# Optimization experiments

Measured on AMD Instinct MI355X. Metric: run time of the kernel, lower is better.

The kernel has to match this reference:

```python
import jax, jax.numpy as jnp
import numpy as np

B, D, E, H, OUT = 4096, 1024, 8, 4096, 1024


def setup_inputs() -> dict:
    key = jax.random.key(0)
    ks = jax.random.split(key, 8)
    s_in = 1.0 / np.sqrt(D)
    s_h = 1.0 / np.sqrt(H)
    return {
        "x": jax.random.normal(ks[0], (B, D), dtype=jnp.float32),
        "Wg": jax.random.uniform(ks[1], (D, E), minval=-s_in, maxval=s_in, dtype=jnp.float32),
        "bg": jnp.zeros((E,), dtype=jnp.float32),
        "W1": jax.random.uniform(ks[2], (E, D, H), minval=-s_in, maxval=s_in, dtype=jnp.float32),
        "b1": jnp.zeros((E, H), dtype=jnp.float32),
        "W2": jax.random.uniform(ks[3], (E, H, OUT), minval=-s_h, maxval=s_h, dtype=jnp.float32),
        "b2": jnp.zeros((E, OUT), dtype=jnp.float32),
        "w_bal": jnp.float32(0.01),
    }


def reference(x, Wg, bg, W1, b1, W2, b2, w_bal):
    # Gating: softmax then top-1 (== argmax of logits)
    gate_logits = x @ Wg + bg                      # [B, E]
    assign = jnp.argmax(gate_logits, axis=1)       # [B] top-1 expert
    onehot = jax.nn.one_hot(assign, E, dtype=x.dtype)  # [B, E] dispatch mask

    # Dense dispatch: run every expert MLP, combine by one-hot (top-1 select).
    # Original returns raw expert output (no gate-prob scaling).
    h = jax.nn.relu(jnp.einsum("bd,edh->ebh", x, W1) + b1[:, None, :])  # [E, B, H]
    y = jnp.einsum("ebh,eho->ebo", h, W2) + b2[:, None, :]              # [E, B, OUT]
    output = jnp.einsum("ebo,be->bo", y, onehot)                        # [B, OUT]

    # Load-balance loss on per-expert token counts
    loads = onehot.sum(axis=0)                     # [E]
    balance_loss = jnp.sum((loads - loads.mean()) ** 2) / E
    return output, balance_loss * w_bal
```

## Files before the change

kernel.cpp:

```cpp
#include <hip/hip_runtime.h>
#include <hip/hip_bf16.h>

typedef unsigned short u16;
typedef __attribute__((ext_vector_type(8))) short bf16x8;
typedef __attribute__((ext_vector_type(4))) float f32x4;

#define BTOK 4096
#define DDIM 1024
#define NEXP 8
#define HDIM 4096
#define ODIM 1024
#define MAXTILES 40
#define MAXROWS (MAXTILES * 128)

__device__ __forceinline__ u16 f2bf(float f) {
  unsigned u = __float_as_uint(f);
  return (u16)((u + 0x7FFFu + ((u >> 16) & 1u)) >> 16);
}
__device__ __forceinline__ u16 cvt_bf(float f) {
  __hip_bfloat16 h = __float2bfloat16(f);
  u16 r;
  __builtin_memcpy(&r, &h, 2);
  return r;
}

__device__ __forceinline__ void gload16(const void* g, void* l) {
  __builtin_amdgcn_global_load_lds(
      (const __attribute__((address_space(1))) void*)g,
      (__attribute__((address_space(3))) void*)l, 16, 0, 0);
}

__global__ __launch_bounds__(256) void init_kernel(int* __restrict__ ctrl,
                                                   int* __restrict__ rowmap) {
  int i = blockIdx.x * 256 + threadIdx.x;
  if (i < 1024)
    ctrl[i] = 0;
  else
    rowmap[i - 1024] = -1;
}

__global__ __launch_bounds__(256) void gate_kernel(
    const float* __restrict__ x, const float* __restrict__ Wg,
    const float* __restrict__ bg, int* __restrict__ assign,
    int* __restrict__ counts) {
  int wave = threadIdx.x >> 6;
  int lane = threadIdx.x & 63;
  int b = blockIdx.x * 4 + wave;
  const float* xr = x + (size_t)b * DDIM;
  double acc[NEXP];
#pragma unroll
  for (int e = 0; e < NEXP; ++e) acc[e] = 0.0;
  for (int d = lane; d < DDIM; d += 64) {
    float xv = xr[d];
    const float4* wrow = (const float4*)(Wg + d * NEXP);
    float4 w0 = wrow[0], w1 = wrow[1];
    acc[0] += (double)xv * (double)w0.x;
    acc[1] += (double)xv * (double)w0.y;
    acc[2] += (double)xv * (double)w0.z;
    acc[3] += (double)xv * (double)w0.w;
    acc[4] += (double)xv * (double)w1.x;
    acc[5] += (double)xv * (double)w1.y;
    acc[6] += (double)xv * (double)w1.z;
    acc[7] += (double)xv * (double)w1.w;
  }
#pragma unroll
  for (int e = 0; e < NEXP; ++e) {
    double v = acc[e];
#pragma unroll
    for (int off = 32; off > 0; off >>= 1) v += __shfl_xor(v, off);
    acc[e] = v;
  }
  if (lane == 0) {
    int best = 0;
    double bv = acc[0] + (double)bg[0];
#pragma unroll
    for (int e = 1; e < NEXP; ++e) {
      double v = acc[e] + (double)bg[e];
      if (v > bv) { bv = v; best = e; }
    }
    assign[b] = best;
    atomicAdd(&counts[best], 1);
  }
}

__global__ void setup_kernel(const int* __restrict__ counts,
                             const float* __restrict__ wbal,
                             int* __restrict__ offp, int* __restrict__ tile_e,
                             int* __restrict__ tile_m, int* __restrict__ meta,
                             float* __restrict__ loss_out) {
  if (threadIdx.x != 0 || blockIdx.x != 0) return;
  int off = 0, nt = 0;
  for (int e = 0; e < NEXP; ++e) {
    offp[e] = off;
    int pc = (counts[e] + 127) & ~127;
    for (int t = 0; t < (pc >> 7); ++t) {
      tile_e[nt] = e;
      tile_m[nt] = off + t * 128;
      ++nt;
    }
    off += pc;
  }
  offp[NEXP] = off;
  meta[0] = nt;
  float mean = (float)BTOK / (float)NEXP;
  float s = 0.f;
  for (int e = 0; e < NEXP; ++e) {
    float d = (float)counts[e] - mean;
    s += d * d;
  }
  loss_out[0] = s / (float)NEXP * wbal[0];
}

__device__ __forceinline__ void transpose_chunk(const float* __restrict__ W,
                                                u16* __restrict__ wt, int K,
                                                int N, int chunk,
                                                float (*lds)[68]) {
  const int t = threadIdx.x;
  const int e = chunk >> 8;
  const int r = chunk & 255;
  const int nK = K >> 6;
  const int kb = (r & (nK - 1)) * 64;
  const int nb0 = (r / nK) * 256;
  const float* src = W + (size_t)e * K * N;
  const int rr = t >> 4, cc = (t & 15) * 4;
  const int n = t & 63, kg = (t >> 6) * 16;
#pragma unroll 1
  for (int s = 0; s < 4; ++s) {
    const int nb = nb0 + s * 64;
#pragma unroll
    for (int p = 0; p < 4; ++p) {
      float4 v =
          *(const float4*)(src + (size_t)(kb + rr + p * 16) * N + nb + cc);
      *(float4*)&lds[rr + p * 16][cc] = v;
    }
    __syncthreads();
    alignas(16) u16 tmp[16];
#pragma unroll
    for (int i = 0; i < 16; ++i) tmp[i] = cvt_bf(lds[kg + i][n]);
    u16* dst = wt + ((size_t)e * N + nb + n) * K + kb + kg;
    *(float4*)dst = *(float4*)&tmp[0];
    *(float4*)(dst + 8) = *(float4*)&tmp[8];
    __syncthreads();
  }
}

__global__ __launch_bounds__(256, 4) void fused_gather_t1(
    const float* __restrict__ x, const int* __restrict__ assign,
    const int* __restrict__ offp, int* __restrict__ fill,
    int* __restrict__ rowmap, u16* __restrict__ xg,
    const float* __restrict__ W1, u16* __restrict__ wt1) {
  __shared__ __align__(16) float tl[64][68];
  const int id = blockIdx.x;
  if (id < BTOK) {
    __shared__ int srow;
    if (threadIdx.x == 0) {
      int e = assign[id];
      int pos = atomicAdd(&fill[e], 1);
      int row = offp[e] + pos;
      rowmap[row] = id;
      srow = row;
    }
    __syncthreads();
    int row = srow;
    float4 v = *(const float4*)(x + (size_t)id * DDIM + threadIdx.x * 4);
    ushort4 o;
    o.x = f2bf(v.x);
    o.y = f2bf(v.y);
    o.z = f2bf(v.z);
    o.w = f2bf(v.w);
    *(ushort4*)(xg + (size_t)row * DDIM + threadIdx.x * 4) = o;
  } else {
    transpose_chunk(W1, wt1, DDIM, HDIM, id - BTOK, tl);
  }
}

template <int MODE>
__device__ __forceinline__ void gemm_core(
    u16* lds, int bx, int by, int bz, const u16* __restrict__ A, int lda,
    const u16* __restrict__ BT, int ldb, int nbRows,
    const float* __restrict__ bias, const int* __restrict__ tile_e,
    const int* __restrict__ tile_m, u16* __restrict__ Hout, int ldn,
    float* __restrict__ P, size_t pStride, int nkt) {
  const int e = tile_e[bx];
  const int m0 = tile_m[bx];
  const int n0 = by * 128;
  const int kOff = bz * nkt * 32;

  const int tid = threadIdx.x;
  const int lane = tid & 63;
  const int wave = tid >> 6;
  const int wr = wave >> 1, wc = wave & 1;
  const int fr = lane & 15;
  const int kqr = lane >> 4;

  const int r0 = tid >> 2, k0 = (tid & 3) ^ ((r0 >> 1) & 3);
  const int r1 = (tid + 256) >> 2, k1 = ((tid + 256) & 3) ^ ((r1 >> 1) & 3);
  const u16* aS0 = A + (size_t)(m0 + r0) * lda + kOff + k0 * 8;
  const u16* aS1 = A + (size_t)(m0 + r1) * lda + kOff + k1 * 8;
  const u16* bPan = BT + ((size_t)e * nbRows + n0) * ldb + kOff;
  const u16* bS0 = bPan + (size_t)r0 * ldb + k0 * 8;
  const u16* bS1 = bPan + (size_t)r1 * ldb + k1 * 8;
  const int dst0 = (tid & ~63) * 8;
  const int dst1 = dst0 + 2048;

  int aOff[4], bOff[4];
#pragma unroll
  for (int i = 0; i < 4; ++i) {
    int r = wr * 64 + i * 16 + fr;
    aOff[i] = (r * 4 + (kqr ^ ((r >> 1) & 3))) * 8;
    int c = wc * 64 + i * 16 + fr;
    bOff[i] = (c * 4 + (kqr ^ ((c >> 1) & 3))) * 8;
  }

  f32x4 acc[4][4];
#pragma unroll
  for (int i = 0; i < 4; ++i)
#pragma unroll
    for (int j = 0; j < 4; ++j)
#pragma unroll
      for (int r = 0; r < 4; ++r) acc[i][j][r] = 0.f;

  auto stage = [&](int c, int kt) {
    const int ko = kt * 32;
    u16* base = lds + c * 8192;
    gload16(aS0 + ko, base + dst0);
    gload16(aS1 + ko, base + dst1);
    gload16(bS0 + ko, base + 4096 + dst0);
    gload16(bS1 + ko, base + 4096 + dst1);
  };
  auto compute = [&](int c) {
    const u16* base = lds + c * 8192;
    bf16x8 af[4], bfr[4];
#pragma unroll
    for (int i = 0; i < 4; ++i) {
      af[i] = *(const bf16x8*)(base + aOff[i]);
      bfr[i] = *(const bf16x8*)(base + 4096 + bOff[i]);
    }
    __builtin_amdgcn_s_setprio(1);
#pragma unroll
    for (int i = 0; i < 4; ++i)
#pragma unroll
      for (int j = 0; j < 4; ++j)
        acc[i][j] = __builtin_amdgcn_mfma_f32_16x16x32_bf16(af[i], bfr[j],
                                                            acc[i][j], 0, 0, 0);
    __builtin_amdgcn_s_setprio(0);
  };

  stage(0, 0);
  int cur = 0;
#pragma unroll 1
  for (int kt = 0; kt < nkt - 1; ++kt) {
    stage(cur ^ 1, kt + 1);
    asm volatile("s_waitcnt vmcnt(4)" ::: "memory");
    __builtin_amdgcn_sched_barrier(0);
    __builtin_amdgcn_s_barrier();
    __builtin_amdgcn_sched_barrier(0);
    compute(cur);
    __builtin_amdgcn_sched_barrier(0);
    __builtin_amdgcn_s_barrier();
    cur ^= 1;
  }
  asm volatile("s_waitcnt vmcnt(0)" ::: "memory");
  __builtin_amdgcn_sched_barrier(0);
  __builtin_amdgcn_s_barrier();
  __builtin_amdgcn_sched_barrier(0);
  compute(cur);

  if constexpr (MODE == 0) {
#pragma unroll
    for (int i = 0; i < 4; ++i) {
      int rbase = m0 + wr * 64 + i * 16 + (lane >> 4) * 4;
#pragma unroll
      for (int j = 0; j < 4; ++j) {
        int col = n0 + wc * 64 + j * 16 + fr;
        float bv = bias[e * ldn + col];
#pragma unroll
        for (int r = 0; r < 4; ++r) {
          float v = acc[i][j][r] + bv;
          v = v > 0.f ? v : 0.f;
          Hout[(size_t)(rbase + r) * ldn + col] = f2bf(v);
        }
      }
    }
  } else {
    float* Pp = P + bz * pStride;
#pragma unroll
    for (int i = 0; i < 4; ++i) {
      int rbase = m0 + wr * 64 + i * 16 + (lane >> 4) * 4;
#pragma unroll
      for (int j = 0; j < 4; ++j) {
        int col = n0 + wc * 64 + j * 16 + fr;
#pragma unroll
        for (int r = 0; r < 4; ++r)
          Pp[(size_t)(rbase + r) * ODIM + col] = acc[i][j][r];
      }
    }
  }
}

__global__ __launch_bounds__(256, 4) void fused_g1_t2(
    const u16* __restrict__ xg, const u16* __restrict__ wt1,
    const float* __restrict__ b1, const float* __restrict__ W2,
    u16* __restrict__ wt2, u16* __restrict__ h, const int* __restrict__ tile_e,
    const int* __restrict__ tile_m, const int* __restrict__ meta) {
  __shared__ __align__(16) char smem[32768];
  const int id = blockIdx.x;
  if (id < 1280) {
    const int wg = (id & 7) * 160 + (id >> 3);
    const int bx = wg % MAXTILES, by = wg / MAXTILES;
    if (bx >= meta[0]) return;
    gemm_core<0>((u16*)smem, bx, by, 0, xg, DDIM, wt1, DDIM, HDIM, b1, tile_e,
                 tile_m, h, HDIM, nullptr, 0, DDIM / 32);
  } else {
    transpose_chunk(W2, wt2, HDIM, ODIM, id - 1280, (float(*)[68])smem);
  }
}

__global__ __launch_bounds__(256, 4) void moe_gemm2(
    const u16* __restrict__ h, const u16* __restrict__ wt2,
    const int* __restrict__ tile_e, const int* __restrict__ tile_m,
    const int* __restrict__ meta, float* __restrict__ P, size_t pStride) {
  __shared__ __align__(16) u16 lds[2 * 8192];
  const int orig = blockIdx.y * MAXTILES + blockIdx.x;
  const int wg = (orig & 7) * 40 + (orig >> 3);
  const int bx = wg % MAXTILES, by = wg / MAXTILES;
  if (bx >= meta[0]) return;
  gemm_core<1>(lds, bx, by, blockIdx.z, h, HDIM, wt2, HDIM, ODIM, nullptr,
               tile_e, tile_m, nullptr, 0, P, pStride, (HDIM / 2) / 32);
}

__global__ __launch_bounds__(256) void reduce_kernel(
    const float* __restrict__ P, size_t pStride, const int* __restrict__ rowmap,
    const int* __restrict__ tile_e, const int* __restrict__ tile_m,
    const int* __restrict__ meta, const float* __restrict__ b2,
    float* __restrict__ out) {
  if ((int)blockIdx.x >= meta[0]) return;
  const int e = tile_e[blockIdx.x];
  const int m0 = tile_m[blockIdx.x];
  const int c0 = blockIdx.y * 128;
#pragma unroll 1
  for (int it = 0; it < 16; ++it) {
    int idx = it * 256 + threadIdx.x;
    int r = idx >> 5, cq = idx & 31;
    int row = m0 + r;
    int tok = rowmap[row];
    if (tok < 0) continue;
    int c = c0 + cq * 4;
    float4 a = *(const float4*)(P + (size_t)row * ODIM + c);
    float4 b = *(const float4*)(P + pStride + (size_t)row * ODIM + c);
    float4 bb = *(const float4*)(b2 + (size_t)e * ODIM + c);
    float4 o;
    o.x = a.x + b.x + bb.x;
    o.y = a.y + b.y + bb.y;
    o.z = a.z + b.z + bb.z;
    o.w = a.w + b.w + bb.w;
    *(float4*)(out + (size_t)tok * ODIM + c) = o;
  }
}

extern "C" void kernel_launch(void* const* d_in, const int* in_sizes, int n_in,
                              void* d_out, int out_size, void* d_ws,
                              size_t ws_size, hipStream_t stream) {
  const float* x = (const float*)d_in[0];
  const float* Wg = (const float*)d_in[1];
  const float* bg = (const float*)d_in[2];
  const float* W1 = (const float*)d_in[3];
  const float* b1 = (const float*)d_in[4];
  const float* W2 = (const float*)d_in[5];
  const float* b2 = (const float*)d_in[6];
  const float* wbal = (const float*)d_in[7];
  float* out = (float*)d_out;

  char* ws = (char*)d_ws;
  int* counts = (int*)(ws + 0);
  int* fill = (int*)(ws + 64);
  int* offp = (int*)(ws + 128);
  int* meta = (int*)(ws + 192);
  int* tile_e = (int*)(ws + 256);
  int* tile_m = (int*)(ws + 512);
  int* assign = (int*)(ws + 4096);
  int* rowmap = (int*)(ws + 20480);
  u16* xg = (u16*)(ws + 65536);
  u16* h = (u16*)(ws + 10551296);
  float* P = (float*)(ws + 52494336);
  u16* wt1 = (u16*)(ws + 94437376);
  u16* wt2 = (u16*)(ws + 161546240);
  const size_t pStride = (size_t)MAXROWS * ODIM;

  init_kernel<<<24, 256, 0, stream>>>((int*)ws, rowmap);
  gate_kernel<<<BTOK / 4, 256, 0, stream>>>(x, Wg, bg, assign, counts);
  setup_kernel<<<1, 64, 0, stream>>>(counts, wbal, offp, tile_e, tile_m, meta,
                                     out + (size_t)BTOK * ODIM);
  fused_gather_t1<<<BTOK + 2048, 256, 0, stream>>>(x, assign, offp, fill,
                                                   rowmap, xg, W1, wt1);
  fused_g1_t2<<<1280 + 2048, 256, 0, stream>>>(xg, wt1, b1, W2, wt2, h, tile_e,
                                               tile_m, meta);
  moe_gemm2<<<dim3(MAXTILES, ODIM / 128, 2), 256, 0, stream>>>(
      h, wt2, tile_e, tile_m, meta, P, pStride);
  reduce_kernel<<<dim3(MAXTILES, ODIM / 128), 256, 0, stream>>>(
      P, pStride, rowmap, tile_e, tile_m, meta, b2, out);
}
```

Before: 356.7 us.

## Triple-buffer GEMM k-loop, split fused kernels, remap XCD tile scheduling

Moves the GEMM core from a two-stage to a three-stage LDS pipeline, prefetching two k-tiles ahead so each iteration needs only one barrier. The previously fused gather/transpose and gemm1/transpose kernels are split into a gather kernel, a combined W1+W2 transpose kernel, and standalone gemm1/gemm2 kernels. The block-to-tile mapping is changed so each XCD handles a contiguous set of N columns. Launch-bounds occupancy hints are dropped and LDS use per block rises to 48KB, which may lower occupancy. Splitting the kernels also gives up the overlap of the transposes with the gather and GEMM1 work.

```diff
diff --git a/kernel.cpp b/kernel.cpp
--- a/kernel.cpp
+++ b/kernel.cpp
@@ -109,6 +109,30 @@
     s += d * d;
   }
   loss_out[0] = s / (float)NEXP * wbal[0];
+}
+
+__global__ __launch_bounds__(256) void gather_kernel(
+    const float* __restrict__ x, const int* __restrict__ assign,
+    const int* __restrict__ offp, int* __restrict__ fill,
+    int* __restrict__ rowmap, u16* __restrict__ xg) {
+  int b = blockIdx.x;
+  __shared__ int srow;
+  if (threadIdx.x == 0) {
+    int e = assign[b];
+    int pos = atomicAdd(&fill[e], 1);
+    int row = offp[e] + pos;
+    rowmap[row] = b;
+    srow = row;
+  }
+  __syncthreads();
+  int row = srow;
+  float4 v = *(const float4*)(x + (size_t)b * DDIM + threadIdx.x * 4);
+  ushort4 o;
+  o.x = f2bf(v.x);
+  o.y = f2bf(v.y);
+  o.z = f2bf(v.z);
+  o.w = f2bf(v.w);
+  *(ushort4*)(xg + (size_t)row * DDIM + threadIdx.x * 4) = o;
 }
 
 __device__ __forceinline__ void transpose_chunk(const float* __restrict__ W,
@@ -144,34 +168,16 @@
   }
 }
 
-__global__ __launch_bounds__(256, 4) void fused_gather_t1(
-    const float* __restrict__ x, const int* __restrict__ assign,
-    const int* __restrict__ offp, int* __restrict__ fill,
-    int* __restrict__ rowmap, u16* __restrict__ xg,
-    const float* __restrict__ W1, u16* __restrict__ wt1) {
+__global__ __launch_bounds__(256) void trans_both(const float* __restrict__ W1,
+                                                  u16* __restrict__ wt1,
+                                                  const float* __restrict__ W2,
+                                                  u16* __restrict__ wt2) {
   __shared__ __align__(16) float tl[64][68];
   const int id = blockIdx.x;
-  if (id < BTOK) {
-    __shared__ int srow;
-    if (threadIdx.x == 0) {
-      int e = assign[id];
-      int pos = atomicAdd(&fill[e], 1);
-      int row = offp[e] + pos;
-      rowmap[row] = id;
-      srow = row;
-    }
-    __syncthreads();
-    int row = srow;
-    float4 v = *(const float4*)(x + (size_t)id * DDIM + threadIdx.x * 4);
-    ushort4 o;
-    o.x = f2bf(v.x);
-    o.y = f2bf(v.y);
-    o.z = f2bf(v.z);
-    o.w = f2bf(v.w);
-    *(ushort4*)(xg + (size_t)row * DDIM + threadIdx.x * 4) = o;
-  } else {
-    transpose_chunk(W1, wt1, DDIM, HDIM, id - BTOK, tl);
-  }
+  if (id < 2048)
+    transpose_chunk(W1, wt1, DDIM, HDIM, id, tl);
+  else
+    transpose_chunk(W2, wt2, HDIM, ODIM, id - 2048, tl);
 }
 
 template <int MODE>
@@ -220,16 +226,16 @@
 #pragma unroll
       for (int r = 0; r < 4; ++r) acc[i][j][r] = 0.f;
 
-  auto stage = [&](int c, int kt) {
+  auto stage = [&](int buf, int kt) {
     const int ko = kt * 32;
-    u16* base = lds + c * 8192;
+    u16* base = lds + buf * 8192;
     gload16(aS0 + ko, base + dst0);
     gload16(aS1 + ko, base + dst1);
     gload16(bS0 + ko, base + 4096 + dst0);
     gload16(bS1 + ko, base + 4096 + dst1);
   };
-  auto compute = [&](int c) {
-    const u16* base = lds + c * 8192;
+  auto compute = [&](int buf) {
+    const u16* base = lds + buf * 8192;
     bf16x8 af[4], bfr[4];
 #pragma unroll
     for (int i = 0; i < 4; ++i) {
@@ -247,24 +253,30 @@
   };
 
   stage(0, 0);
-  int cur = 0;
-#pragma unroll 1
-  for (int kt = 0; kt < nkt - 1; ++kt) {
-    stage(cur ^ 1, kt + 1);
-    asm volatile("s_waitcnt vmcnt(4)" ::: "memory");
-    __builtin_amdgcn_sched_barrier(0);
-    __builtin_amdgcn_s_barrier();
-    __builtin_amdgcn_sched_barrier(0);
-    compute(cur);
-    __builtin_amdgcn_sched_barrier(0);
-    __builtin_amdgcn_s_barrier();
-    cur ^= 1;
-  }
-  asm volatile("s_waitcnt vmcnt(0)" ::: "memory");
+  stage(1, 1);
   __builtin_amdgcn_sched_barrier(0);
+  asm volatile("s_waitcnt vmcnt(4)" ::: "memory");
   __builtin_amdgcn_s_barrier();
   __builtin_amdgcn_sched_barrier(0);
-  compute(cur);
+
+  int cur = 0, nst = 2;
+#pragma unroll 1
+  for (int t = 0; t < nkt; ++t) {
+    const bool more = (t + 2 < nkt);
+    if (more) stage(nst, t + 2);
+    compute(cur);
+    cur = (cur == 2) ? 0 : cur + 1;
+    nst = (nst == 2) ? 0 : nst + 1;
+    if (t + 1 < nkt) {
+      __builtin_amdgcn_sched_barrier(0);
+      if (more)
+        asm volatile("s_waitcnt vmcnt(4)" ::: "memory");
+      else
+        asm volatile("s_waitcnt vmcnt(0)" ::: "memory");
+      __builtin_amdgcn_s_barrier();
+      __builtin_amdgcn_sched_barrier(0);
+    }
+  }
 
   if constexpr (MODE == 0) {
 #pragma unroll
@@ -298,32 +310,32 @@
   }
 }
 
-__global__ __launch_bounds__(256, 4) void fused_g1_t2(
+__global__ __launch_bounds__(256) void moe_gemm1(
     const u16* __restrict__ xg, const u16* __restrict__ wt1,
-    const float* __restrict__ b1, const float* __restrict__ W2,
-    u16* __restrict__ wt2, u16* __restrict__ h, const int* __restrict__ tile_e,
-    const int* __restrict__ tile_m, const int* __restrict__ meta) {
-  __shared__ __align__(16) char smem[32768];
-  const int id = blockIdx.x;
-  if (id < 1280) {
-    const int wg = (id & 7) * 160 + (id >> 3);
-    const int bx = wg % MAXTILES, by = wg / MAXTILES;
-    if (bx >= meta[0]) return;
-    gemm_core<0>((u16*)smem, bx, by, 0, xg, DDIM, wt1, DDIM, HDIM, b1, tile_e,
-                 tile_m, h, HDIM, nullptr, 0, DDIM / 32);
-  } else {
-    transpose_chunk(W2, wt2, HDIM, ODIM, id - 1280, (float(*)[68])smem);
-  }
-}
-
-__global__ __launch_bounds__(256, 4) void moe_gemm2(
+    const float* __restrict__ b1, const int* __restrict__ tile_e,
+    const int* __restrict__ tile_m, const int* __restrict__ meta,
+    u16* __restrict__ h) {
+  __shared__ __align__(16) u16 lds[3 * 8192];
+  const int orig = blockIdx.y * MAXTILES + blockIdx.x;
+  const int xcd = orig & 7;
+  const int idx = orig >> 3;
+  const int bx = idx % MAXTILES;
+  const int by = xcd * 4 + idx / MAXTILES;
+  if (bx >= meta[0]) return;
+  gemm_core<0>(lds, bx, by, 0, xg, DDIM, wt1, DDIM, HDIM, b1, tile_e, tile_m,
+               h, HDIM, nullptr, 0, DDIM / 32);
+}
+
+__global__ __launch_bounds__(256) void moe_gemm2(
     const u16* __restrict__ h, const u16* __restrict__ wt2,
     const int* __restrict__ tile_e, const int* __restrict__ tile_m,
     const int* __restrict__ meta, float* __restrict__ P, size_t pStride) {
-  __shared__ __align__(16) u16 lds[2 * 8192];
+  __shared__ __align__(16) u16 lds[3 * 8192];
   const int orig = blockIdx.y * MAXTILES + blockIdx.x;
-  const int wg = (orig & 7) * 40 + (orig >> 3);
-  const int bx = wg % MAXTILES, by = wg / MAXTILES;
+  const int xcd = orig & 7;
+  const int idx = orig >> 3;
+  const int bx = idx;
+  const int by = xcd;
   if (bx >= meta[0]) return;
   gemm_core<1>(lds, bx, by, blockIdx.z, h, HDIM, wt2, HDIM, ODIM, nullptr,
                tile_e, tile_m, nullptr, 0, P, pStride, (HDIM / 2) / 32);
@@ -391,10 +403,11 @@
   gate_kernel<<<BTOK / 4, 256, 0, stream>>>(x, Wg, bg, assign, counts);
   setup_kernel<<<1, 64, 0, stream>>>(counts, wbal, offp, tile_e, tile_m, meta,
                                      out + (size_t)BTOK * ODIM);
-  fused_gather_t1<<<BTOK + 2048, 256, 0, stream>>>(x, assign, offp, fill,
-                                                   rowmap, xg, W1, wt1);
-  fused_g1_t2<<<1280 + 2048, 256, 0, stream>>>(xg, wt1, b1, W2, wt2, h, tile_e,
-                                               tile_m, meta);
+  gather_kernel<<<BTOK, 256, 0, stream>>>(x, assign, offp, fill, rowmap, xg);
+  trans_both<<<4096, 256, 0, stream>>>(W1, wt1, W2, wt2);
+
+  moe_gemm1<<<dim3(MAXTILES, HDIM / 128), 256, 0, stream>>>(
+      xg, wt1, b1, tile_e, tile_m, meta, h);
   moe_gemm2<<<dim3(MAXTILES, ODIM / 128, 2), 256, 0, stream>>>(
       h, wt2, tile_e, tile_m, meta, P, pStride);
   reduce_kernel<<<dim3(MAXTILES, ODIM / 128), 256, 0, stream>>>(
```

After: 360.7 us. About the same (+1.1%).
